# Kernel tuning notes

Measured on AMD Instinct MI355X. Metric: run time of the kernel, lower is better.

The kernel has to match this reference:

```python
import jax, jax.numpy as jnp
import numpy as np

HEIGHT = 450.0
# aspect_ratio = [input_h/450, input_w/450, 1] with input_shape=(224,224,3)
ASPECT = (224.0 / 450.0, 224.0 / 450.0, 1.0)

N_VERTS = 53215          # num_landmarks (full BFM mesh)
N_ROWS = 3 * N_VERTS     # 159645
EXP_DIM = 29
SHP_DIM = 199


def setup_inputs() -> dict:
    key = jax.random.key(0)
    ks = jax.random.split(key, 6)
    return {
        "pose_3DMM": jax.random.normal(ks[0], (1, 12), jnp.float32),
        "alpha_exp": jax.random.normal(ks[1], (1, EXP_DIM), jnp.float32),
        "alpha_shp": jax.random.normal(ks[2], (1, SHP_DIM), jnp.float32),
        "u_base": jax.random.normal(ks[3], (N_ROWS, 1), jnp.float32),
        "w_exp_base": jax.random.normal(ks[4], (N_ROWS, EXP_DIM), jnp.float32),
        "w_shp_base": jax.random.normal(ks[5], (N_ROWS, SHP_DIM), jnp.float32),
    }


def _transform_matrix(pose_3DMM, height):
    # pose_3DMM: (B, 12) -> (B, 3, 4); original code only supports B == 1
    Tm = pose_3DMM.reshape(-1, 3, 4)
    R = Tm[0, :, :3]                       # (3, 3)
    t_all = Tm[:, :, 3]                    # (B, 3)
    s = jnp.sum(t_all[-1])                 # scalar scale = sum of last translation (as in source)
    t = t_all[0] * jnp.array([1.0, 1.0, 0.0], Tm.dtype)  # zero out z (diag([1,1,0]) @ t)
    T = jnp.zeros((4, 4), Tm.dtype).at[:3, :3].set(R).at[3, 3].set(1.0)
    S = jnp.diag(jnp.concatenate([jnp.full((3,), s, Tm.dtype), jnp.ones((1,), Tm.dtype)]))
    T = S @ T
    M = jnp.eye(4, dtype=Tm.dtype).at[:3, 3].set(t)
    T = M @ T
    H = jnp.eye(4, dtype=Tm.dtype).at[1, 1].set(-1.0).at[1, 3].set(height)
    return H @ T                           # (4, 4)


def reference(pose_3DMM, alpha_exp, alpha_shp, u_base, w_exp_base, w_shp_base):
    # vertices: (B, 3N, 1) = u + W_exp @ a_exp + W_shp @ a_shp (broadcast batched matmul)
    vertices = u_base + (jnp.matmul(w_exp_base, alpha_exp[..., None])
                         + jnp.matmul(w_shp_base, alpha_shp[..., None]))
    B = vertices.shape[0]
    v = vertices.reshape(B, -1, 3)                        # (B, N, 3)
    T = _transform_matrix(pose_3DMM, jnp.asarray(HEIGHT, v.dtype))
    ones = jnp.ones((B, v.shape[1], 1), v.dtype)
    homo = jnp.concatenate([v, ones], axis=-1)            # (B, N, 4)
    img = jnp.matmul(homo, T.T)[:, :, :3]                 # (B, N, 3)
    return img * jnp.asarray(ASPECT, img.dtype)
```

## Files before the change

### kernel.cpp

```cpp
#include <hip/hip_runtime.h>

#define N_VERTS 53215
#define EXP_DIM 29
#define SHP_DIM 199
#define HEIGHT_F 450.0f
#define ASPECT_XY (224.0f / 450.0f)

__global__ __launch_bounds__(192) void pca_transform_kernel(
    const float* __restrict__ pose,
    const float* __restrict__ alpha_exp,
    const float* __restrict__ alpha_shp,
    const float* __restrict__ u_base,
    const float* __restrict__ w_exp,
    const float* __restrict__ w_shp,
    float* __restrict__ out)
{
    const int vert = blockIdx.x;
    const int wave = threadIdx.x >> 6;
    const int lane = threadIdx.x & 63;
    const int row  = vert * 3 + wave;

    const float* __restrict__ srow = w_shp + (size_t)row * SHP_DIM;
    float sum = 0.0f;
    #pragma unroll 4
    for (int k = lane; k < SHP_DIM; k += 64)
        sum += srow[k] * alpha_shp[k];

    const float* __restrict__ erow = w_exp + (size_t)row * EXP_DIM;
    if (lane < EXP_DIM)
        sum += erow[lane] * alpha_exp[lane];

    #pragma unroll
    for (int off = 32; off > 0; off >>= 1)
        sum += __shfl_xor(sum, off, 64);

    __shared__ float v[3];
    if (lane == 0)
        v[wave] = u_base[row] + sum;
    __syncthreads();

    if (threadIdx.x == 0) {
        const float vx = v[0], vy = v[1], vz = v[2];
        const float tx = pose[3], ty = pose[7];
        const float s  = pose[3] + pose[7] + pose[11];
        const float ox = s * (pose[0] * vx + pose[1] * vy + pose[2]  * vz) + tx;
        const float oy = -(s * (pose[4] * vx + pose[5] * vy + pose[6] * vz) + ty) + HEIGHT_F;
        const float oz = s * (pose[8] * vx + pose[9] * vy + pose[10] * vz);
        float* o = out + (size_t)vert * 3;
        o[0] = ox * ASPECT_XY;
        o[1] = oy * ASPECT_XY;
        o[2] = oz;
    }
}

extern "C" void kernel_launch(void* const* d_in, const int* in_sizes, int n_in,
                              void* d_out, int out_size, void* d_ws, size_t ws_size,
                              hipStream_t stream) {
    const float* pose      = (const float*)d_in[0];
    const float* alpha_exp = (const float*)d_in[1];
    const float* alpha_shp = (const float*)d_in[2];
    const float* u_base    = (const float*)d_in[3];
    const float* w_exp     = (const float*)d_in[4];
    const float* w_shp     = (const float*)d_in[5];
    float* out = (float*)d_out;

    pca_transform_kernel<<<N_VERTS, 192, 0, stream>>>(
        pose, alpha_exp, alpha_shp, u_base, w_exp, w_shp, out);
}
```

Baseline: 218.8 us.

## Assign one wave per vertex with grid-stride loop and hoisted coefficients

Replaces the one-block-per-vertex design (three waves plus shared memory and a barrier) with a persistent grid of 2048 blocks in which each wave processes whole vertices in a grid-stride loop. Pose and alpha coefficients are loaded once per thread into registers, and each wave issues all twelve shape loads plus the expression loads for the three rows before reducing them together with interleaved shuffles. The intent is to remove per-block launch, barrier and shared-memory overhead and to put more memory loads in flight on this bandwidth-bound matrix-vector product. Only lane 0 writes the output. It adds register pressure from the many outstanding loads.

```diff
diff --git a/kernel.cpp b/kernel.cpp
--- a/kernel.cpp
+++ b/kernel.cpp
@@ -6,7 +6,7 @@
 #define HEIGHT_F 450.0f
 #define ASPECT_XY (224.0f / 450.0f)
 
-__global__ __launch_bounds__(192) void pca_transform_kernel(
+__global__ __launch_bounds__(256, 8) void pca_transform_kernel(
     const float* __restrict__ pose,
     const float* __restrict__ alpha_exp,
     const float* __restrict__ alpha_shp,
@@ -15,41 +15,57 @@
     const float* __restrict__ w_shp,
     float* __restrict__ out)
 {
-    const int vert = blockIdx.x;
-    const int wave = threadIdx.x >> 6;
-    const int lane = threadIdx.x & 63;
-    const int row  = vert * 3 + wave;
+    const int lane   = threadIdx.x & 63;
+    const int gwave  = (int)((blockIdx.x * blockDim.x + threadIdx.x) >> 6);
+    const int nwaves = (int)((gridDim.x * blockDim.x) >> 6);
 
-    const float* __restrict__ srow = w_shp + (size_t)row * SHP_DIM;
-    float sum = 0.0f;
-    #pragma unroll 4
-    for (int k = lane; k < SHP_DIM; k += 64)
-        sum += srow[k] * alpha_shp[k];
+    const float p0 = pose[0], p1 = pose[1], p2  = pose[2],  p3  = pose[3];
+    const float p4 = pose[4], p5 = pose[5], p6  = pose[6],  p7  = pose[7];
+    const float p8 = pose[8], p9 = pose[9], p10 = pose[10], p11 = pose[11];
+    const float s  = p3 + p7 + p11;
 
-    const float* __restrict__ erow = w_exp + (size_t)row * EXP_DIM;
-    if (lane < EXP_DIM)
-        sum += erow[lane] * alpha_exp[lane];
+    const int  k3 = (lane < 7)  ? lane + 192 : 198;
+    const int  ke = (lane < EXP_DIM) ? lane : (EXP_DIM - 1);
+    const float a0 = alpha_shp[lane];
+    const float a1 = alpha_shp[lane + 64];
+    const float a2 = alpha_shp[lane + 128];
+    const float a3 = (lane < 7) ? alpha_shp[k3] : 0.0f;
+    const float ae = (lane < EXP_DIM) ? alpha_exp[ke] : 0.0f;
 
-    #pragma unroll
-    for (int off = 32; off > 0; off >>= 1)
-        sum += __shfl_xor(sum, off, 64);
+    for (int v = gwave; v < N_VERTS; v += nwaves) {
+        const float* __restrict__ sx_p = w_shp + (size_t)(3 * v) * SHP_DIM;
+        const float* __restrict__ sy_p = sx_p + SHP_DIM;
+        const float* __restrict__ sz_p = sy_p + SHP_DIM;
+        const float* __restrict__ ex_p = w_exp + (size_t)(3 * v) * EXP_DIM;
 
-    __shared__ float v[3];
-    if (lane == 0)
-        v[wave] = u_base[row] + sum;
-    __syncthreads();
+        const float x0 = sx_p[lane], x1 = sx_p[lane + 64], x2 = sx_p[lane + 128], x3 = sx_p[k3];
+        const float y0 = sy_p[lane], y1 = sy_p[lane + 64], y2 = sy_p[lane + 128], y3 = sy_p[k3];
+        const float z0 = sz_p[lane], z1 = sz_p[lane + 64], z2 = sz_p[lane + 128], z3 = sz_p[k3];
+        const float xe = ex_p[ke], ye = ex_p[EXP_DIM + ke], ze = ex_p[2 * EXP_DIM + ke];
 
-    if (threadIdx.x == 0) {
-        const float vx = v[0], vy = v[1], vz = v[2];
-        const float tx = pose[3], ty = pose[7];
-        const float s  = pose[3] + pose[7] + pose[11];
-        const float ox = s * (pose[0] * vx + pose[1] * vy + pose[2]  * vz) + tx;
-        const float oy = -(s * (pose[4] * vx + pose[5] * vy + pose[6] * vz) + ty) + HEIGHT_F;
-        const float oz = s * (pose[8] * vx + pose[9] * vy + pose[10] * vz);
-        float* o = out + (size_t)vert * 3;
-        o[0] = ox * ASPECT_XY;
-        o[1] = oy * ASPECT_XY;
-        o[2] = oz;
+        float sx = x0 * a0 + x1 * a1 + x2 * a2 + x3 * a3 + xe * ae;
+        float sy = y0 * a0 + y1 * a1 + y2 * a2 + y3 * a3 + ye * ae;
+        float sz = z0 * a0 + z1 * a1 + z2 * a2 + z3 * a3 + ze * ae;
+
+        #pragma unroll
+        for (int off = 32; off > 0; off >>= 1) {
+            sx += __shfl_xor(sx, off, 64);
+            sy += __shfl_xor(sy, off, 64);
+            sz += __shfl_xor(sz, off, 64);
+        }
+
+        const float vx = sx + u_base[3 * v + 0];
+        const float vy = sy + u_base[3 * v + 1];
+        const float vz = sz + u_base[3 * v + 2];
+
+        const float ox = ASPECT_XY * (s * (p0 * vx + p1 * vy + p2  * vz) + p3);
+        const float oy = ASPECT_XY * (HEIGHT_F - (s * (p4 * vx + p5 * vy + p6 * vz) + p7));
+        const float oz = s * (p8 * vx + p9 * vy + p10 * vz);
+
+        if (lane == 0) {
+            float* o = out + (size_t)v * 3;
+            o[0] = ox; o[1] = oy; o[2] = oz;
+        }
     }
 }
 
@@ -64,6 +80,6 @@
     const float* w_shp     = (const float*)d_in[5];
     float* out = (float*)d_out;
 
-    pca_transform_kernel<<<N_VERTS, 192, 0, stream>>>(
+    pca_transform_kernel<<<2048, 256, 0, stream>>>(
         pose, alpha_exp, alpha_shp, u_base, w_exp, w_shp, out);
 }
```

Result: faster. 207.3 us (-5.3%).

## Split into vectorized strip GEMV kernel and separate pose transform kernel

Applied to the files above, without the earlier changes.

Replaces the one-block-per-vertex kernel with a grid-stride GEMV in which each group of four lanes handles one row. Rows are read with aligned float4 loads, and the alpha coefficients are pre-shifted into registers so each row's misalignment is absorbed. The pose transform moves to a second lightweight kernel that reads intermediate vertices from workspace. This targets the poor memory efficiency and high block count of the old kernel, at the cost of an extra launch, a workspace round trip, and a masked scalar tail path for the last strip.

```diff
diff --git a/kernel.cpp b/kernel.cpp
--- a/kernel.cpp
+++ b/kernel.cpp
@@ -1,56 +1,125 @@
 #include <hip/hip_runtime.h>
 
 #define N_VERTS 53215
+#define N_ROWS  (3 * N_VERTS)
 #define EXP_DIM 29
 #define SHP_DIM 199
+#define TOT_S   (N_ROWS * SHP_DIM)
+#define TOT_E   (N_ROWS * EXP_DIM)
+#define STRIPS  ((N_ROWS + 15) / 16)
 #define HEIGHT_F 450.0f
 #define ASPECT_XY (224.0f / 450.0f)
 
-__global__ __launch_bounds__(192) void pca_transform_kernel(
-    const float* __restrict__ pose,
+__global__ __launch_bounds__(256) void pca_gemv_kernel(
     const float* __restrict__ alpha_exp,
     const float* __restrict__ alpha_shp,
     const float* __restrict__ u_base,
     const float* __restrict__ w_exp,
     const float* __restrict__ w_shp,
+    float* __restrict__ y)
+{
+    __shared__ float als[212];
+    __shared__ float ale[40];
+
+    const int t = threadIdx.x;
+    if (t < 212) als[t] = (t >= 4 && t < 4 + SHP_DIM) ? alpha_shp[t - 4] : 0.0f;
+    if (t >= 212 && t < 252) {
+        const int u = t - 212;
+        ale[u] = (u >= 4 && u < 4 + EXP_DIM) ? alpha_exp[u - 4] : 0.0f;
+    }
+    __syncthreads();
+
+    const int lane = t & 63;
+    const int q    = lane & 3;
+    const int r16  = lane >> 2;
+    const int wid  = (int)((blockIdx.x * blockDim.x + t) >> 6);
+    const int nw   = (int)((gridDim.x * blockDim.x) >> 6);
+
+    const int shiftS = (3 * r16) & 3;
+    const int shiftE = r16 & 3;
+
+    float aS[13][4], aE[2][4];
+    #pragma unroll
+    for (int j = 0; j < 13; ++j)
+        #pragma unroll
+        for (int k = 0; k < 4; ++k)
+            aS[j][k] = als[4 - shiftS + 4 * q + 16 * j + k];
+    #pragma unroll
+    for (int je = 0; je < 2; ++je)
+        #pragma unroll
+        for (int k = 0; k < 4; ++k)
+            aE[je][k] = ale[4 - shiftE + 4 * q + 16 * je + k];
+
+    for (int s = wid; s < STRIPS; s += nw) {
+        const int rowv = s * 16 + r16;
+        const int rowc = (rowv < N_ROWS) ? rowv : (N_ROWS - 1);
+        const int b   = rowc * SHP_DIM;
+        const int f0  = b - (b & 3);
+        const int be  = rowc * EXP_DIM;
+        const int f0e = be - (be & 3);
+
+        float sum = 0.0f;
+        if (s != STRIPS - 1) {
+            #pragma unroll
+            for (int j = 0; j < 13; ++j) {
+                const float4 w = *(const float4*)(w_shp + f0 + 4 * q + 16 * j);
+                sum += w.x * aS[j][0] + w.y * aS[j][1] + w.z * aS[j][2] + w.w * aS[j][3];
+            }
+            #pragma unroll
+            for (int je = 0; je < 2; ++je) {
+                const float4 e = *(const float4*)(w_exp + f0e + 4 * q + 16 * je);
+                sum += e.x * aE[je][0] + e.y * aE[je][1] + e.z * aE[je][2] + e.w * aE[je][3];
+            }
+        } else {
+            #pragma unroll
+            for (int j = 0; j < 13; ++j) {
+                const int base = f0 + 4 * q + 16 * j;
+                #pragma unroll
+                for (int k = 0; k < 4; ++k) {
+                    const int idx = base + k;
+                    sum += w_shp[idx < TOT_S ? idx : (TOT_S - 1)] * aS[j][k];
+                }
+            }
+            #pragma unroll
+            for (int je = 0; je < 2; ++je) {
+                const int base = f0e + 4 * q + 16 * je;
+                #pragma unroll
+                for (int k = 0; k < 4; ++k) {
+                    const int idx = base + k;
+                    sum += w_exp[idx < TOT_E ? idx : (TOT_E - 1)] * aE[je][k];
+                }
+            }
+        }
+
+        sum += __shfl_xor(sum, 1, 64);
+        sum += __shfl_xor(sum, 2, 64);
+
+        if (q == 0 && rowv < N_ROWS)
+            y[rowv] = sum + u_base[rowv];
+    }
+}
+
+__global__ __launch_bounds__(256) void pca_pose_kernel(
+    const float* __restrict__ pose,
+    const float* __restrict__ y,
     float* __restrict__ out)
 {
-    const int vert = blockIdx.x;
-    const int wave = threadIdx.x >> 6;
-    const int lane = threadIdx.x & 63;
-    const int row  = vert * 3 + wave;
+    const int v = blockIdx.x * blockDim.x + threadIdx.x;
+    if (v >= N_VERTS) return;
 
-    const float* __restrict__ srow = w_shp + (size_t)row * SHP_DIM;
-    float sum = 0.0f;
-    #pragma unroll 4
-    for (int k = lane; k < SHP_DIM; k += 64)
-        sum += srow[k] * alpha_shp[k];
+    const float vx = y[3 * v + 0];
+    const float vy = y[3 * v + 1];
+    const float vz = y[3 * v + 2];
 
-    const float* __restrict__ erow = w_exp + (size_t)row * EXP_DIM;
-    if (lane < EXP_DIM)
-        sum += erow[lane] * alpha_exp[lane];
+    const float p0 = pose[0], p1 = pose[1], p2  = pose[2],  p3  = pose[3];
+    const float p4 = pose[4], p5 = pose[5], p6  = pose[6],  p7  = pose[7];
+    const float p8 = pose[8], p9 = pose[9], p10 = pose[10], p11 = pose[11];
+    const float s  = p3 + p7 + p11;
 
-    #pragma unroll
-    for (int off = 32; off > 0; off >>= 1)
-        sum += __shfl_xor(sum, off, 64);
-
-    __shared__ float v[3];
-    if (lane == 0)
-        v[wave] = u_base[row] + sum;
-    __syncthreads();
-
-    if (threadIdx.x == 0) {
-        const float vx = v[0], vy = v[1], vz = v[2];
-        const float tx = pose[3], ty = pose[7];
-        const float s  = pose[3] + pose[7] + pose[11];
-        const float ox = s * (pose[0] * vx + pose[1] * vy + pose[2]  * vz) + tx;
-        const float oy = -(s * (pose[4] * vx + pose[5] * vy + pose[6] * vz) + ty) + HEIGHT_F;
-        const float oz = s * (pose[8] * vx + pose[9] * vy + pose[10] * vz);
-        float* o = out + (size_t)vert * 3;
-        o[0] = ox * ASPECT_XY;
-        o[1] = oy * ASPECT_XY;
-        o[2] = oz;
-    }
+    float* o = out + (size_t)v * 3;
+    o[0] = ASPECT_XY * (s * (p0 * vx + p1 * vy + p2  * vz) + p3);
+    o[1] = ASPECT_XY * (HEIGHT_F - (s * (p4 * vx + p5 * vy + p6 * vz) + p7));
+    o[2] = s * (p8 * vx + p9 * vy + p10 * vz);
 }
 
 extern "C" void kernel_launch(void* const* d_in, const int* in_sizes, int n_in,
@@ -63,7 +132,10 @@
     const float* w_exp     = (const float*)d_in[4];
     const float* w_shp     = (const float*)d_in[5];
     float* out = (float*)d_out;
+    float* y   = (float*)d_ws;
 
-    pca_transform_kernel<<<N_VERTS, 192, 0, stream>>>(
-        pose, alpha_exp, alpha_shp, u_base, w_exp, w_shp, out);
+    pca_gemv_kernel<<<1248, 256, 0, stream>>>(
+        alpha_exp, alpha_shp, u_base, w_exp, w_shp, y);
+
+    pca_pose_kernel<<<(N_VERTS + 255) / 256, 256, 0, stream>>>(pose, y, out);
 }
```

Measured after the change: 215.5 us. About the same (-1.5%).
